# Optimization experiments

Hardware: AMD Instinct MI355X
Metric: run time of the kernel (lower is better)

The kernel has to match this reference:

```python
import jax, jax.numpy as jnp
import numpy as np

N_DATA = 128      # number of datasets (process conditions)
SEG_LEN = 131072  # thickness points per dataset
N_MAT = 8         # number of distinct materials
N_MATP = 8        # material params: Sigma0, BetaD, Ea, Mfda, Di, A0, B0, l0
N_PROCP = 5       # process params: SigmaC, K0, alpha1, L0, GrainSize_200
RGAS = 8.314      # gas constant, J/(mol K)


def setup_inputs() -> dict:
    key = jax.random.key(0)
    k1, k2, k3, k4 = jax.random.split(key, 4)
    # thickness points: sorted within each dataset segment, scaled to [0, 1]
    x = jax.random.uniform(k1, (N_DATA, SEG_LEN), dtype=jnp.float32)
    x_scaled = jnp.sort(x, axis=1).reshape(-1)
    # process conditions [R, T, P, Melting_T]
    pc = jax.random.uniform(k2, (N_DATA, 4), dtype=jnp.float32)
    R = 0.05 + pc[:, 0]            # deposition rate
    T = 300.0 + 300.0 * pc[:, 1]   # temperature (K)
    P = 0.1 + pc[:, 2]             # pressure
    material_index = jnp.sort(jax.random.randint(k3, (N_DATA,), 0, N_MAT, dtype=jnp.int32))
    melting_T = 1000.0 + 100.0 * material_index.astype(jnp.float32)
    process_c = jnp.stack([R, T, P, melting_T], axis=1)
    # learned raw parameters (pre-sigmoid) and bounds
    n_params = N_MAT * N_MATP + N_DATA * N_PROCP  # 704
    raw_params = 0.5 * jax.random.normal(k4, (n_params,), dtype=jnp.float32)
    para_lb = jnp.full((n_params,), 0.1, dtype=jnp.float32)
    para_ub = jnp.full((n_params,), 2.0, dtype=jnp.float32)
    # MinMaxScaler surrogates: [x_data_min, x_data_max, y_data_min, y_data_max], feature_range=(0,1)
    scaler_params = jnp.array([0.5, 500.0, -50.0, 50.0], dtype=jnp.float32)
    fit_index = jnp.repeat(jnp.arange(1, N_DATA + 1, dtype=jnp.int32), SEG_LEN)
    return {
        'x_scaled': x_scaled, 'process_c': process_c, 'raw_params': raw_params,
        'para_lb': para_lb, 'para_ub': para_ub, 'scaler_params': scaler_params,
        'fit_index': fit_index, 'material_index': material_index,
    }


def _stress(tp, R, T, P, SigmaC, alpha1, L0, G200, Sigma0, BetaD, Ea, Mfda, Di, A0, B0, l0):
    """Kinetic stress equation (Chason-type). tp: [N, L-1]; params broadcast [N, 1]."""
    Lg = G200 * (tp / 200.0 + 1e-3) ** alpha1 + L0      # grain size evolution
    D = Di * jnp.exp(-Ea / (RGAS * T))                   # thermally activated diffusivity
    beta = BetaD * D / (R * Lg + 1e-9)                   # kinetic competition factor
    sigma_ss = (SigmaC - Mfda * P + (Sigma0 / Lg) * beta) / (1.0 + beta)
    return sigma_ss + A0 * jnp.exp(-tp / (B0 * l0 + 1e-9))  # steady-state + transient


def reference(x_scaled, process_c, raw_params, para_lb, para_ub, scaler_params,
              fit_index, material_index):
    n_data = process_c.shape[0]
    seg = x_scaled.shape[0] // n_data
    # unscale parameters: sigmoid -> [lb, ub]
    xv = jax.nn.sigmoid(raw_params) * (para_ub - para_lb) + para_lb
    materials = xv[:N_MAT * N_MATP].reshape(N_MAT, N_MATP)
    process = xv[N_MAT * N_MATP:].reshape(n_data, N_PROCP)
    x_min, x_max, y_min, y_max = scaler_params[0], scaler_params[1], scaler_params[2], scaler_params[3]
    # inverse MinMax transform of thickness (feature_range = (0, 1))
    t = (x_scaled * (x_max - x_min) + x_min).reshape(n_data, seg)  # [N, L]
    SigmaC, K0, alpha1, L0, G200 = (process[:, i:i + 1] for i in range(5))
    mat = materials[material_index]  # [N, 8] gather per-dataset material params
    Sigma0, BetaD, Ea, Mfda, Di, A0, B0, l0 = (mat[:, i:i + 1] for i in range(8))
    R, T, P = process_c[:, 0:1], process_c[:, 1:2], process_c[:, 2:3]
    # Euler integration: Fit[j+1] = Fit[j] + stress(t[j]) * dT  ==  K0 + cumsum
    s = _stress(t[:, :-1], R, T, P, SigmaC, alpha1, L0, G200,
                Sigma0, BetaD, Ea, Mfda, Di, A0, B0, l0)   # [N, L-1]
    dT = jnp.diff(t, axis=1)                                # [N, L-1]
    fit = jnp.concatenate([K0, K0 + jnp.cumsum(s * dT, axis=1)], axis=1).reshape(-1)
    # forward MinMax transform of stress-thickness (feature_range = (0, 1))
    return (fit - y_min) / (y_max - y_min)
```

## Files before the change

kernel.cpp:

```cpp
#include <hip/hip_runtime.h>

#define N_DATA   128
#define SEG_LEN  131072
#define NPROD    (SEG_LEN - 1)
#define N_MAT    8
#define N_MATP   8
#define N_PROCP  5
#define RGAS     8.314f

#define NCH      64
#define CHUNK    2048
#define TPB      256
#define EPT      8

typedef float nt4 __attribute__((ext_vector_type(4)));

__device__ __forceinline__ float stress_s(float t,
    float alpha1, float L0, float G200, float Sigma0, float A0,
    float inv_tau, float cbd, float base_num, float R) {
  float Lg  = G200 * __expf(alpha1 * __logf(t * (1.0f / 200.0f) + 0.001f)) + L0;
  float u   = R * Lg + 1e-9f;
  float num = base_num * u * Lg + Sigma0 * cbd;
  float den = Lg * (u + cbd);
  float sigma_ss = num * __builtin_amdgcn_rcpf(den);
  return sigma_ss + A0 * __expf(-t * inv_tau);
}

__global__ __launch_bounds__(TPB) void k1_sums(
    const float* __restrict__ x,
    const float* __restrict__ pc, const float* __restrict__ raw,
    const float* __restrict__ lb, const float* __restrict__ ub,
    const float* __restrict__ sc, const int* __restrict__ mat_idx,
    float* __restrict__ chunksum) {
  __shared__ float pv[13];
  __shared__ float ws4[4];

  int b   = blockIdx.x;
  int row = b >> 6;
  int ch  = b & (NCH - 1);
  int tid = threadIdx.x;
  int lane = tid & 63, wv = tid >> 6;

  long rowbase = (long)row * SEG_LEN;
  int  gb = ch * CHUNK + tid * EPT;
  const float* xp = x + rowbase + gb;
  float4 a  = *(const float4*)xp;
  float4 bq = *(const float4*)(xp + 4);
  float  xn = (gb + EPT < SEG_LEN) ? xp[EPT] : 0.0f;

  if (tid < 13) {
    int idx = (tid < 5) ? (N_MAT * N_MATP + row * N_PROCP + tid)
                        : (mat_idx[row] * N_MATP + (tid - 5));
    float s = 1.0f / (1.0f + __expf(-raw[idx]));
    pv[tid] = s * (ub[idx] - lb[idx]) + lb[idx];
  }
  __syncthreads();

  float SigmaC = pv[0], alpha1 = pv[2], L0 = pv[3], G200 = pv[4];
  float Sigma0 = pv[5], BetaD = pv[6], Ea = pv[7], Mfda = pv[8], Di = pv[9];
  float A0 = pv[10], B0 = pv[11], l0 = pv[12];
  float R = pc[row * 4 + 0], T = pc[row * 4 + 1], P = pc[row * 4 + 2];
  float cbd      = BetaD * Di * __expf(-Ea / (RGAS * T));
  float base_num = SigmaC - Mfda * P;
  float inv_tau  = 1.0f / (B0 * l0 + 1e-9f);
  float x_min = sc[0], x_sc = sc[1] - sc[0];

  float tv[9];
  tv[0] = a.x  * x_sc + x_min; tv[1] = a.y  * x_sc + x_min;
  tv[2] = a.z  * x_sc + x_min; tv[3] = a.w  * x_sc + x_min;
  tv[4] = bq.x * x_sc + x_min; tv[5] = bq.y * x_sc + x_min;
  tv[6] = bq.z * x_sc + x_min; tv[7] = bq.w * x_sc + x_min;
  tv[8] = xn   * x_sc + x_min;

  float sum = 0.0f;
#pragma unroll
  for (int k = 0; k < EPT; k++) {
    if (gb + k < NPROD) {
      float s = stress_s(tv[k], alpha1, L0, G200, Sigma0, A0, inv_tau, cbd, base_num, R);
      sum += s * (tv[k + 1] - tv[k]);
    }
  }

#pragma unroll
  for (int d = 32; d > 0; d >>= 1) sum += __shfl_down(sum, d);
  if (lane == 0) ws4[wv] = sum;
  __syncthreads();
  if (tid == 0) chunksum[b] = ws4[0] + ws4[1] + ws4[2] + ws4[3];
}

__global__ __launch_bounds__(TPB) void k2_write(
    const float* __restrict__ x,
    const float* __restrict__ pc, const float* __restrict__ raw,
    const float* __restrict__ lb, const float* __restrict__ ub,
    const float* __restrict__ sc, const int* __restrict__ mat_idx,
    const float* __restrict__ chunksum,
    float* __restrict__ out) {
  __shared__ float pv[13];
  __shared__ float wtot[4];

  int b   = blockIdx.x;
  int row = b >> 6;
  int ch  = b & (NCH - 1);
  int tid = threadIdx.x;
  int lane = tid & 63, wv = tid >> 6;

  long rowbase = (long)row * SEG_LEN;
  int  gb = ch * CHUNK + tid * EPT;
  const float* xp = x + rowbase + gb;
  float4 a  = *(const float4*)xp;
  float4 bq = *(const float4*)(xp + 4);
  float  xn = (gb + EPT < SEG_LEN) ? xp[EPT] : 0.0f;
  float csv = chunksum[(row << 6) | lane];

  if (tid < 13) {
    int idx = (tid < 5) ? (N_MAT * N_MATP + row * N_PROCP + tid)
                        : (mat_idx[row] * N_MATP + (tid - 5));
    float s = 1.0f / (1.0f + __expf(-raw[idx]));
    pv[tid] = s * (ub[idx] - lb[idx]) + lb[idx];
  }

  float cincl = csv;
#pragma unroll
  for (int d = 1; d < 64; d <<= 1) {
    float n = __shfl_up(cincl, d);
    if (lane >= d) cincl += n;
  }
  float choff = __shfl(cincl - csv, ch);

  __syncthreads();
  float SigmaC = pv[0], K0 = pv[1], alpha1 = pv[2], L0 = pv[3], G200 = pv[4];
  float Sigma0 = pv[5], BetaD = pv[6], Ea = pv[7], Mfda = pv[8], Di = pv[9];
  float A0 = pv[10], B0 = pv[11], l0 = pv[12];
  float R = pc[row * 4 + 0], T = pc[row * 4 + 1], P = pc[row * 4 + 2];
  float cbd      = BetaD * Di * __expf(-Ea / (RGAS * T));
  float base_num = SigmaC - Mfda * P;
  float inv_tau  = 1.0f / (B0 * l0 + 1e-9f);
  float x_min = sc[0], x_sc = sc[1] - sc[0];
  float y_min = sc[2], inv_yr = 1.0f / (sc[3] - sc[2]);

  float tv[9];
  tv[0] = a.x  * x_sc + x_min; tv[1] = a.y  * x_sc + x_min;
  tv[2] = a.z  * x_sc + x_min; tv[3] = a.w  * x_sc + x_min;
  tv[4] = bq.x * x_sc + x_min; tv[5] = bq.y * x_sc + x_min;
  tv[6] = bq.z * x_sc + x_min; tv[7] = bq.w * x_sc + x_min;
  tv[8] = xn   * x_sc + x_min;

  float pref[EPT];
  float run = 0.0f;
#pragma unroll
  for (int k = 0; k < EPT; k++) {
    float p = 0.0f;
    if (gb + k < NPROD) {
      float s = stress_s(tv[k], alpha1, L0, G200, Sigma0, A0, inv_tau, cbd, base_num, R);
      p = s * (tv[k + 1] - tv[k]);
    }
    run += p;
    pref[k] = run;
  }

  float incl = run;
#pragma unroll
  for (int d = 1; d < 64; d <<= 1) {
    float n = __shfl_up(incl, d);
    if (lane >= d) incl += n;
  }
  if (lane == 63) wtot[wv] = incl;
  __syncthreads();
  float low = 0.0f;
#pragma unroll
  for (int w = 0; w < 4; w++) low += (w < wv) ? wtot[w] : 0.0f;

  float base = K0 + choff + (incl - run) + low;
  nt4 o0, o1;
  o0.x = (base           - y_min) * inv_yr;
  o0.y = (base + pref[0] - y_min) * inv_yr;
  o0.z = (base + pref[1] - y_min) * inv_yr;
  o0.w = (base + pref[2] - y_min) * inv_yr;
  o1.x = (base + pref[3] - y_min) * inv_yr;
  o1.y = (base + pref[4] - y_min) * inv_yr;
  o1.z = (base + pref[5] - y_min) * inv_yr;
  o1.w = (base + pref[6] - y_min) * inv_yr;
  nt4* op = (nt4*)(out + rowbase + gb);
  __builtin_nontemporal_store(o0, op);
  __builtin_nontemporal_store(o1, op + 1);
}

extern "C" void kernel_launch(void* const* d_in, const int* in_sizes, int n_in,
                              void* d_out, int out_size, void* d_ws, size_t ws_size,
                              hipStream_t stream) {
  const float* x_scaled  = (const float*)d_in[0];
  const float* process_c = (const float*)d_in[1];
  const float* raw       = (const float*)d_in[2];
  const float* lb        = (const float*)d_in[3];
  const float* ub        = (const float*)d_in[4];
  const float* sc        = (const float*)d_in[5];
  const int*   mat_idx   = (const int*)d_in[7];
  float* out = (float*)d_out;
  float* chunksum = (float*)d_ws;

  k1_sums<<<N_DATA * NCH, TPB, 0, stream>>>(
      x_scaled, process_c, raw, lb, ub, sc, mat_idx, chunksum);
  k2_write<<<N_DATA * NCH, TPB, 0, stream>>>(
      x_scaled, process_c, raw, lb, ub, sc, mat_idx, chunksum, out);
}
```

Measured before the change: 180.1 us.

## Fuse two-pass scan into single-pass chained scan with flagged atomic chunk sums

Replaces the separate reduce kernel and write kernel with one kernel. Each block publishes its chunk total together with a ready flag in a 64-bit word, then spin-waits on the flags of earlier chunks in the same row to get its offset. A small init kernel clears the flags. This removes the second read of the input and the second stress evaluation. The cost is spin-waiting, which depends on blocks being scheduled roughly in order and could deadlock if earlier blocks never get to run.

```diff
diff --git a/kernel.cpp b/kernel.cpp
--- a/kernel.cpp
+++ b/kernel.cpp
@@ -12,6 +12,7 @@
 #define CHUNK    2048
 #define TPB      256
 #define EPT      8
+#define NBLK     (N_DATA * NCH)
 
 typedef float nt4 __attribute__((ext_vector_type(4)));
 
@@ -26,14 +27,20 @@
   return sigma_ss + A0 * __expf(-t * inv_tau);
 }
 
-__global__ __launch_bounds__(TPB) void k1_sums(
+__global__ __launch_bounds__(TPB) void k0_init(unsigned long long* __restrict__ cs) {
+  cs[blockIdx.x * TPB + threadIdx.x] = 0ull;
+}
+
+__global__ __launch_bounds__(TPB) void k_scan(
     const float* __restrict__ x,
     const float* __restrict__ pc, const float* __restrict__ raw,
     const float* __restrict__ lb, const float* __restrict__ ub,
     const float* __restrict__ sc, const int* __restrict__ mat_idx,
-    float* __restrict__ chunksum) {
+    unsigned long long* __restrict__ cs,
+    float* __restrict__ out) {
   __shared__ float pv[13];
-  __shared__ float ws4[4];
+  __shared__ float wtot[4];
+  __shared__ float choff_s;
 
   int b   = blockIdx.x;
   int row = b >> 6;
@@ -56,78 +63,6 @@
   }
   __syncthreads();
 
-  float SigmaC = pv[0], alpha1 = pv[2], L0 = pv[3], G200 = pv[4];
-  float Sigma0 = pv[5], BetaD = pv[6], Ea = pv[7], Mfda = pv[8], Di = pv[9];
-  float A0 = pv[10], B0 = pv[11], l0 = pv[12];
-  float R = pc[row * 4 + 0], T = pc[row * 4 + 1], P = pc[row * 4 + 2];
-  float cbd      = BetaD * Di * __expf(-Ea / (RGAS * T));
-  float base_num = SigmaC - Mfda * P;
-  float inv_tau  = 1.0f / (B0 * l0 + 1e-9f);
-  float x_min = sc[0], x_sc = sc[1] - sc[0];
-
-  float tv[9];
-  tv[0] = a.x  * x_sc + x_min; tv[1] = a.y  * x_sc + x_min;
-  tv[2] = a.z  * x_sc + x_min; tv[3] = a.w  * x_sc + x_min;
-  tv[4] = bq.x * x_sc + x_min; tv[5] = bq.y * x_sc + x_min;
-  tv[6] = bq.z * x_sc + x_min; tv[7] = bq.w * x_sc + x_min;
-  tv[8] = xn   * x_sc + x_min;
-
-  float sum = 0.0f;
-#pragma unroll
-  for (int k = 0; k < EPT; k++) {
-    if (gb + k < NPROD) {
-      float s = stress_s(tv[k], alpha1, L0, G200, Sigma0, A0, inv_tau, cbd, base_num, R);
-      sum += s * (tv[k + 1] - tv[k]);
-    }
-  }
-
-#pragma unroll
-  for (int d = 32; d > 0; d >>= 1) sum += __shfl_down(sum, d);
-  if (lane == 0) ws4[wv] = sum;
-  __syncthreads();
-  if (tid == 0) chunksum[b] = ws4[0] + ws4[1] + ws4[2] + ws4[3];
-}
-
-__global__ __launch_bounds__(TPB) void k2_write(
-    const float* __restrict__ x,
-    const float* __restrict__ pc, const float* __restrict__ raw,
-    const float* __restrict__ lb, const float* __restrict__ ub,
-    const float* __restrict__ sc, const int* __restrict__ mat_idx,
-    const float* __restrict__ chunksum,
-    float* __restrict__ out) {
-  __shared__ float pv[13];
-  __shared__ float wtot[4];
-
-  int b   = blockIdx.x;
-  int row = b >> 6;
-  int ch  = b & (NCH - 1);
-  int tid = threadIdx.x;
-  int lane = tid & 63, wv = tid >> 6;
-
-  long rowbase = (long)row * SEG_LEN;
-  int  gb = ch * CHUNK + tid * EPT;
-  const float* xp = x + rowbase + gb;
-  float4 a  = *(const float4*)xp;
-  float4 bq = *(const float4*)(xp + 4);
-  float  xn = (gb + EPT < SEG_LEN) ? xp[EPT] : 0.0f;
-  float csv = chunksum[(row << 6) | lane];
-
-  if (tid < 13) {
-    int idx = (tid < 5) ? (N_MAT * N_MATP + row * N_PROCP + tid)
-                        : (mat_idx[row] * N_MATP + (tid - 5));
-    float s = 1.0f / (1.0f + __expf(-raw[idx]));
-    pv[tid] = s * (ub[idx] - lb[idx]) + lb[idx];
-  }
-
-  float cincl = csv;
-#pragma unroll
-  for (int d = 1; d < 64; d <<= 1) {
-    float n = __shfl_up(cincl, d);
-    if (lane >= d) cincl += n;
-  }
-  float choff = __shfl(cincl - csv, ch);
-
-  __syncthreads();
   float SigmaC = pv[0], K0 = pv[1], alpha1 = pv[2], L0 = pv[3], G200 = pv[4];
   float Sigma0 = pv[5], BetaD = pv[6], Ea = pv[7], Mfda = pv[8], Di = pv[9];
   float A0 = pv[10], B0 = pv[11], l0 = pv[12];
@@ -166,6 +101,32 @@
   }
   if (lane == 63) wtot[wv] = incl;
   __syncthreads();
+
+  if (tid == 0) {
+    float tot = wtot[0] + wtot[1] + wtot[2] + wtot[3];
+    unsigned long long u = (1ull << 32) |
+        (unsigned long long)__float_as_uint(tot);
+    __hip_atomic_store(cs + b, u, __ATOMIC_RELAXED, __HIP_MEMORY_SCOPE_AGENT);
+  }
+
+  if (tid < 64) {
+    float v = 0.0f;
+    int l = tid;
+    if (l < ch) {
+      const unsigned long long* p = cs + ((row << 6) | l);
+      unsigned long long u;
+      do {
+        u = __hip_atomic_load(p, __ATOMIC_RELAXED, __HIP_MEMORY_SCOPE_AGENT);
+      } while ((u >> 32) == 0ull);
+      v = __uint_as_float((unsigned)u);
+    }
+#pragma unroll
+    for (int d = 32; d > 0; d >>= 1) v += __shfl_down(v, d);
+    if (tid == 0) choff_s = v;
+  }
+  __syncthreads();
+
+  float choff = choff_s;
   float low = 0.0f;
 #pragma unroll
   for (int w = 0; w < 4; w++) low += (w < wv) ? wtot[w] : 0.0f;
@@ -196,10 +157,9 @@
   const float* sc        = (const float*)d_in[5];
   const int*   mat_idx   = (const int*)d_in[7];
   float* out = (float*)d_out;
-  float* chunksum = (float*)d_ws;
+  unsigned long long* cs = (unsigned long long*)d_ws;
 
-  k1_sums<<<N_DATA * NCH, TPB, 0, stream>>>(
-      x_scaled, process_c, raw, lb, ub, sc, mat_idx, chunksum);
-  k2_write<<<N_DATA * NCH, TPB, 0, stream>>>(
-      x_scaled, process_c, raw, lb, ub, sc, mat_idx, chunksum, out);
+  k0_init<<<NBLK / TPB, TPB, 0, stream>>>(cs);
+  k_scan<<<NBLK, TPB, 0, stream>>>(
+      x_scaled, process_c, raw, lb, ub, sc, mat_idx, cs, out);
 }
```

Result: slower. 189.3 us (+5.1%).
